# Performance work log

Hardware: AMD Instinct MI355X
Metric: run time of the kernel (lower is better)

## Reference

```python
import jax, jax.numpy as jnp
import numpy as np

B, S, E, U = 4, 512, 512, 256

def setup_inputs() -> dict:
    key = jax.random.key(0)
    k1, k2, k3, k4 = jax.random.split(key, 4)
    h1 = jax.random.normal(k1, (B, S, E), dtype=jnp.float32)
    h2 = jax.random.normal(k2, (B, S, E), dtype=jnp.float32)
    # glorot-ish scaled weights
    w = jax.random.normal(k3, (2 * E, U), dtype=jnp.float32) * (2.0 / (2 * E + U)) ** 0.5
    b1 = jnp.zeros((U,), dtype=jnp.float32)
    v = jax.random.normal(k4, (U, 1), dtype=jnp.float32) * (2.0 / (U + 1)) ** 0.5
    b2 = jnp.zeros((1,), dtype=jnp.float32)
    return {"h1": h1, "h2": h2, "w": w, "b1": b1, "v": v, "b2": b2}

def reference(h1, h2, w, b1, v, b2):
    # Original: for each query step i, concat([h1, repeat(h2[:,i])]) @ w.
    # Split w so the concat-matmul becomes two separate projections:
    #   concat([h1_j, h2_i]) @ w == h1_j @ w1 + h2_i @ w2
    E_ = h1.shape[-1]
    w1, w2 = w[:E_], w[E_:]
    key_pre = jnp.einsum('bje,eu->bju', h1, w1)   # [B,Sk,U]
    qry_pre = jnp.einsum('bie,eu->biu', h2, w2)   # [B,Sq,U]
    # energy: [B,Sq,Sk,U]
    t = jnp.tanh(qry_pre[:, :, None, :] + key_pre[:, None, :, :] + b1)
    scores = jnp.einsum('biju,uo->bij', t, v) + b2[0]  # [B,Sq,Sk]
    p = jax.nn.softmax(scores, axis=-1)                # softmax over keys j
    # context per query: sum_j p[b,i,j] * h1[b,j]
    return jnp.einsum('bij,bje->bie', p, h1)           # [B,S,E]
```

## Files before the change

kernel.cpp:

```cpp
#include <hip/hip_runtime.h>
#include <hip/hip_bf16.h>

#define B_ 4
#define S_ 512
#define E_ 512
#define U_ 256

#define KC 2.885390081777927f

#if __has_builtin(__builtin_amdgcn_exp2f)
#define EXP2F(x) __builtin_amdgcn_exp2f(x)
#else
#define EXP2F(x) __exp2f(x)
#endif
#if __has_builtin(__builtin_amdgcn_rcpf)
#define RCPF(x) __builtin_amdgcn_rcpf(x)
#else
#define RCPF(x) (1.0f / (x))
#endif

typedef __attribute__((ext_vector_type(8))) short bf16x8;
typedef __attribute__((ext_vector_type(4))) float f32x4;

__device__ __forceinline__ unsigned short bf16rn(float x) {
    unsigned int u = __float_as_uint(x);
    u = (u + 0x7FFFu + ((u >> 16) & 1u)) >> 16;
    return (unsigned short)u;
}
__device__ __forceinline__ void splitT(float x, short* hi, short* lo) {
    const unsigned u = __float_as_uint(x);
    *hi = (short)(u >> 16);
    const float hf = __uint_as_float(u & 0xFFFF0000u);
    *lo = (short)(__float_as_uint(x - hf) >> 16);
}

__global__ __launch_bounds__(256) void prep_gemm(
    const float* __restrict__ h1, const float* __restrict__ h2,
    const float* __restrict__ w, const float* __restrict__ b1,
    float* __restrict__ keySt, float* __restrict__ qryS,
    bf16x8* __restrict__ h1c)
{
    __shared__ unsigned short WhiL[2][16][64][8];
    __shared__ unsigned short WloL[2][16][64][8];

    const int tid = threadIdx.x;
    const int bid = blockIdx.x;

    if (bid < 512) {
        const int z = bid >> 8, ngg = (bid >> 5) & 7, mq = bid & 31;

        const int r8 = tid >> 5, ul = tid & 31;
        const int ntc = ul >> 4, l16c = ul & 15;
        const float* __restrict__ Wp = w + (size_t)z * E_ * U_ + ngg * 32 + ul;
#pragma unroll 4
        for (int it = 0; it < 64; ++it) {
            const int k = it * 8 + r8;
            short h, l;
            splitT(Wp[(size_t)k * U_] * KC, &h, &l);
            const int kc = k >> 5, quad = (k >> 3) & 3, jj = k & 7;
            WhiL[ntc][kc][quad * 16 + l16c][jj] = (unsigned short)h;
            WloL[ntc][kc][quad * 16 + l16c][jj] = (unsigned short)l;
        }
        __syncthreads();

        const int wv = tid >> 6, lane = tid & 63;
        const int quad = lane >> 4, l16 = lane & 15;
        const int m0 = (mq * 4 + wv) * 16;
        const float* __restrict__ Arow = (z ? h2 : h1) + (size_t)(m0 + l16) * E_;

        f32x4 acc[2];
        acc[0] = (f32x4){0.f, 0.f, 0.f, 0.f};
        acc[1] = (f32x4){0.f, 0.f, 0.f, 0.f};

        for (int kc = 0; kc < 16; ++kc) {
            const int kb = kc * 32 + quad * 8;
            const float4 x0 = *(const float4*)&Arow[kb];
            const float4 x1 = *(const float4*)&Arow[kb + 4];
            const float xs[8] = {x0.x, x0.y, x0.z, x0.w, x1.x, x1.y, x1.z, x1.w};
            bf16x8 ah, al;
#pragma unroll
            for (int j = 0; j < 8; ++j) {
                short h, l; splitT(xs[j], &h, &l);
                ah[j] = h; al[j] = l;
            }
#pragma unroll
            for (int nt = 0; nt < 2; ++nt) {
                const bf16x8 bh = *(const bf16x8*)&WhiL[nt][kc][lane][0];
                const bf16x8 bl = *(const bf16x8*)&WloL[nt][kc][lane][0];
                acc[nt] = __builtin_amdgcn_mfma_f32_16x16x32_bf16(ah, bh, acc[nt], 0, 0, 0);
                acc[nt] = __builtin_amdgcn_mfma_f32_16x16x32_bf16(ah, bl, acc[nt], 0, 0, 0);
                acc[nt] = __builtin_amdgcn_mfma_f32_16x16x32_bf16(al, bh, acc[nt], 0, 0, 0);
            }
        }

        if (z == 0) {
            const int b = m0 >> 9;
            const int j0 = (m0 & (S_ - 1)) + quad * 4;
#pragma unroll
            for (int nt = 0; nt < 2; ++nt) {
                const int u = (ngg * 2 + nt) * 16 + l16;
                *(float4*)&keySt[((size_t)b * U_ + u) * S_ + j0] =
                    make_float4(acc[nt][0], acc[nt][1], acc[nt][2], acc[nt][3]);
            }
        } else {
            const int row = m0 + quad * 4;
#pragma unroll
            for (int nt = 0; nt < 2; ++nt) {
                const int u = (ngg * 2 + nt) * 16 + l16;
                const float bias = KC * b1[u];
#pragma unroll
                for (int r = 0; r < 4; ++r)
                    qryS[(size_t)(row + r) * U_ + u] = acc[nt][r] + bias;
            }
        }
    } else {
        const int s = (bid - 512) * 256 + tid;
        const int lane = s & 63, kc = (s >> 6) & 15, et = (s >> 10) & 31, b = s >> 15;
        const int quad = lane >> 4, l16 = lane & 15;
        const float* __restrict__ src =
            h1 + ((size_t)b * S_ + kc * 32 + quad * 8) * E_ + et * 16 + l16;
        bf16x8 c;
#pragma unroll
        for (int j = 0; j < 8; ++j)
            c[j] = (short)bf16rn(src[(size_t)j * E_]);
        h1c[s] = c;
    }
}

__device__ __forceinline__ float quadTerm(float a0, float a1, float a2, float a3,
                                          float4 vq, float acc) {
    const float F1 = EXP2F(a0) + 1.f;
    const float F2 = EXP2F(a1) + 1.f;
    const float F3 = EXP2F(a2) + 1.f;
    const float F4 = EXP2F(a3) + 1.f;
    const float P12 = F1 * F2, P34 = F3 * F4;
    const float n12 = fmaf(vq.y, F1, vq.x * F2);
    const float n34 = fmaf(vq.w, F3, vq.z * F4);
    const float num = fmaf(n34, P12, n12 * P34);
    return fmaf(num, RCPF(P12 * P34), acc);
}

__global__ __launch_bounds__(512) void scores_kernel(
    const float* __restrict__ keySt, const float* __restrict__ qryS,
    const float* __restrict__ v, unsigned short* __restrict__ Pp)
{
    const int i0 = blockIdx.x * 4;
    const int b = blockIdx.y;
    const int t = threadIdx.x;
    const int wv = t >> 6;

    __shared__ float ssm[8][4];

    const float4* __restrict__ q0v = (const float4*)(qryS + ((size_t)b * S_ + i0) * U_);
    const float4* __restrict__ q1v = q0v + (U_ / 4);
    const float4* __restrict__ q2v = q0v + 2 * (U_ / 4);
    const float4* __restrict__ q3v = q0v + 3 * (U_ / 4);
    const float4* __restrict__ vv4 = (const float4*)v;
    const float* __restrict__ kb = keySt + (size_t)b * U_ * S_ + t;

    float a0 = 0.f, a1 = 0.f, a2 = 0.f, a3 = 0.f;
#pragma unroll 4
    for (int ub = 0; ub < U_ / 4; ++ub) {
        const float4 vq = vv4[ub];
        const float k0 = kb[(size_t)(ub * 4 + 0) * S_];
        const float k1 = kb[(size_t)(ub * 4 + 1) * S_];
        const float k2 = kb[(size_t)(ub * 4 + 2) * S_];
        const float k3 = kb[(size_t)(ub * 4 + 3) * S_];
        const float4 q0 = q0v[ub], q1 = q1v[ub], q2 = q2v[ub], q3 = q3v[ub];
        a0 = quadTerm(q0.x + k0, q0.y + k1, q0.z + k2, q0.w + k3, vq, a0);
        a1 = quadTerm(q1.x + k0, q1.y + k1, q1.z + k2, q1.w + k3, vq, a1);
        a2 = quadTerm(q2.x + k0, q2.y + k1, q2.z + k2, q2.w + k3, vq, a2);
        a3 = quadTerm(q3.x + k0, q3.y + k1, q3.z + k2, q3.w + k3, vq, a3);
    }

    const float p0 = EXP2F(-a0 * KC);
    const float p1 = EXP2F(-a1 * KC);
    const float p2 = EXP2F(-a2 * KC);
    const float p3 = EXP2F(-a3 * KC);
    float s0 = p0, s1 = p1, s2 = p2, s3 = p3;
#pragma unroll
    for (int off = 1; off < 64; off <<= 1) {
        s0 += __shfl_xor(s0, off, 64);
        s1 += __shfl_xor(s1, off, 64);
        s2 += __shfl_xor(s2, off, 64);
        s3 += __shfl_xor(s3, off, 64);
    }
    if ((t & 63) == 0) {
        ssm[wv][0] = s0; ssm[wv][1] = s1; ssm[wv][2] = s2; ssm[wv][3] = s3;
    }
    __syncthreads();
    s0 = ssm[0][0]; s1 = ssm[0][1]; s2 = ssm[0][2]; s3 = ssm[0][3];
#pragma unroll
    for (int k = 1; k < 8; ++k) {
        s0 += ssm[k][0]; s1 += ssm[k][1]; s2 += ssm[k][2]; s3 += ssm[k][3];
    }
    const float r0 = RCPF(s0), r1 = RCPF(s1), r2 = RCPF(s2), r3 = RCPF(s3);

    const int itile = i0 >> 4;
    const int base = (itile * 16 + (t >> 5)) * 64 + (((t >> 3) & 3) << 4);
    unsigned short* __restrict__ pb = Pp + (size_t)b * S_ * S_;
    const int io = i0 & 15, jo = t & 7;
    pb[((base + io + 0) << 3) + jo] = bf16rn(p0 * r0);
    pb[((base + io + 1) << 3) + jo] = bf16rn(p1 * r1);
    pb[((base + io + 2) << 3) + jo] = bf16rn(p2 * r2);
    pb[((base + io + 3) << 3) + jo] = bf16rn(p3 * r3);
}

__global__ __launch_bounds__(256) void pv_gemm(
    const unsigned short* __restrict__ Pp, const bf16x8* __restrict__ h1c,
    float* __restrict__ out)
{
    const int tid = threadIdx.x;
    const int wv = tid >> 6, lane = tid & 63;
    const int quad = lane >> 4, l16 = lane & 15;
    const int wt = blockIdx.x * 4 + wv;
    const int b = wt >> 8, rem = wt & 255;
    const int it = rem >> 3, eg = rem & 7;

    const bf16x8* __restrict__ Ab =
        (const bf16x8*)(Pp + (size_t)b * S_ * S_) + (it * 16) * 64 + lane;
    const bf16x8* __restrict__ Bb =
        h1c + ((b * 32 + eg * 4) * 16) * 64 + lane;

    f32x4 acc[4];
#pragma unroll
    for (int i = 0; i < 4; ++i) acc[i] = (f32x4){0.f, 0.f, 0.f, 0.f};

    for (int kc = 0; kc < 16; ++kc) {
        const bf16x8 a8 = Ab[kc * 64];
#pragma unroll
        for (int n = 0; n < 4; ++n) {
            const bf16x8 b8 = Bb[(n * 16 + kc) * 64];
            acc[n] = __builtin_amdgcn_mfma_f32_16x16x32_bf16(a8, b8, acc[n], 0, 0, 0);
        }
    }

    const int i = it * 16 + quad * 4;
#pragma unroll
    for (int n = 0; n < 4; ++n) {
        const int e = (eg * 4 + n) * 16 + l16;
        float* __restrict__ ob = out + ((size_t)b * S_ + i) * E_ + e;
#pragma unroll
        for (int r = 0; r < 4; ++r)
            ob[(size_t)r * E_] = acc[n][r];
    }
}

extern "C" void kernel_launch(void* const* d_in, const int* in_sizes, int n_in,
                              void* d_out, int out_size, void* d_ws, size_t ws_size,
                              hipStream_t stream) {
    const float* h1 = (const float*)d_in[0];
    const float* h2 = (const float*)d_in[1];
    const float* w  = (const float*)d_in[2];
    const float* b1 = (const float*)d_in[3];
    const float* v  = (const float*)d_in[4];
    float* out = (float*)d_out;

    char* ws = (char*)d_ws;
    float* keySt = (float*)ws;                 ws += 2u << 20;
    float* qryS  = (float*)ws;                 ws += 2u << 20;
    unsigned short* Pp = (unsigned short*)ws;  ws += 2u << 20;
    bf16x8* h1c = (bf16x8*)ws;

    prep_gemm<<<dim3(1024), dim3(256), 0, stream>>>(h1, h2, w, b1, keySt, qryS, h1c);
    scores_kernel<<<dim3(S_ / 4, B_), dim3(512), 0, stream>>>(keySt, qryS, v, Pp);
    pv_gemm<<<dim3(256), dim3(256), 0, stream>>>(Pp, h1c, out);
}
```

Measured before the change: 137.8 us.

## Split GEMM tiles finer for more blocks and prefetch keys in scores loop

The projection GEMM now gives each block one 16-wide column tile instead of two, doubling its grid. The PV GEMM gives each wave one 16-column output tile instead of four, quadrupling its grid. The scores kernel software-prefetches the next four key values one iteration ahead. The aim is better occupancy and latency hiding on the GPU, at the cost of reloading the A operands more often and recomputing the W split per block.

```diff
diff --git a/kernel.cpp b/kernel.cpp
--- a/kernel.cpp
+++ b/kernel.cpp
@@ -40,26 +40,25 @@
     float* __restrict__ keySt, float* __restrict__ qryS,
     bf16x8* __restrict__ h1c)
 {
-    __shared__ unsigned short WhiL[2][16][64][8];
-    __shared__ unsigned short WloL[2][16][64][8];
+    __shared__ unsigned short WhiL[16][64][8];
+    __shared__ unsigned short WloL[16][64][8];
 
     const int tid = threadIdx.x;
     const int bid = blockIdx.x;
 
-    if (bid < 512) {
-        const int z = bid >> 8, ngg = (bid >> 5) & 7, mq = bid & 31;
-
-        const int r8 = tid >> 5, ul = tid & 31;
-        const int ntc = ul >> 4, l16c = ul & 15;
-        const float* __restrict__ Wp = w + (size_t)z * E_ * U_ + ngg * 32 + ul;
+    if (bid < 1024) {
+        const int z = bid >> 9, ng = (bid >> 5) & 15, mq = bid & 31;
+
+        const int l16c = tid & 15, r16 = tid >> 4;
+        const float* __restrict__ Wp = w + (size_t)z * E_ * U_ + ng * 16 + l16c;
 #pragma unroll 4
-        for (int it = 0; it < 64; ++it) {
-            const int k = it * 8 + r8;
+        for (int it = 0; it < 32; ++it) {
+            const int k = it * 16 + r16;
             short h, l;
             splitT(Wp[(size_t)k * U_] * KC, &h, &l);
             const int kc = k >> 5, quad = (k >> 3) & 3, jj = k & 7;
-            WhiL[ntc][kc][quad * 16 + l16c][jj] = (unsigned short)h;
-            WloL[ntc][kc][quad * 16 + l16c][jj] = (unsigned short)l;
+            WhiL[kc][quad * 16 + l16c][jj] = (unsigned short)h;
+            WloL[kc][quad * 16 + l16c][jj] = (unsigned short)l;
         }
         __syncthreads();
 
@@ -68,9 +67,7 @@
         const int m0 = (mq * 4 + wv) * 16;
         const float* __restrict__ Arow = (z ? h2 : h1) + (size_t)(m0 + l16) * E_;
 
-        f32x4 acc[2];
-        acc[0] = (f32x4){0.f, 0.f, 0.f, 0.f};
-        acc[1] = (f32x4){0.f, 0.f, 0.f, 0.f};
+        f32x4 acc = (f32x4){0.f, 0.f, 0.f, 0.f};
 
         for (int kc = 0; kc < 16; ++kc) {
             const int kb = kc * 32 + quad * 8;
@@ -83,38 +80,28 @@
                 short h, l; splitT(xs[j], &h, &l);
                 ah[j] = h; al[j] = l;
             }
-#pragma unroll
-            for (int nt = 0; nt < 2; ++nt) {
-                const bf16x8 bh = *(const bf16x8*)&WhiL[nt][kc][lane][0];
-                const bf16x8 bl = *(const bf16x8*)&WloL[nt][kc][lane][0];
-                acc[nt] = __builtin_amdgcn_mfma_f32_16x16x32_bf16(ah, bh, acc[nt], 0, 0, 0);
-                acc[nt] = __builtin_amdgcn_mfma_f32_16x16x32_bf16(ah, bl, acc[nt], 0, 0, 0);
-                acc[nt] = __builtin_amdgcn_mfma_f32_16x16x32_bf16(al, bh, acc[nt], 0, 0, 0);
-            }
+            const bf16x8 bh = *(const bf16x8*)&WhiL[kc][lane][0];
+            const bf16x8 bl = *(const bf16x8*)&WloL[kc][lane][0];
+            acc = __builtin_amdgcn_mfma_f32_16x16x32_bf16(ah, bh, acc, 0, 0, 0);
+            acc = __builtin_amdgcn_mfma_f32_16x16x32_bf16(ah, bl, acc, 0, 0, 0);
+            acc = __builtin_amdgcn_mfma_f32_16x16x32_bf16(al, bh, acc, 0, 0, 0);
         }
 
+        const int u = ng * 16 + l16;
         if (z == 0) {
             const int b = m0 >> 9;
             const int j0 = (m0 & (S_ - 1)) + quad * 4;
-#pragma unroll
-            for (int nt = 0; nt < 2; ++nt) {
-                const int u = (ngg * 2 + nt) * 16 + l16;
-                *(float4*)&keySt[((size_t)b * U_ + u) * S_ + j0] =
-                    make_float4(acc[nt][0], acc[nt][1], acc[nt][2], acc[nt][3]);
-            }
+            *(float4*)&keySt[((size_t)b * U_ + u) * S_ + j0] =
+                make_float4(acc[0], acc[1], acc[2], acc[3]);
         } else {
             const int row = m0 + quad * 4;
-#pragma unroll
-            for (int nt = 0; nt < 2; ++nt) {
-                const int u = (ngg * 2 + nt) * 16 + l16;
-                const float bias = KC * b1[u];
-#pragma unroll
-                for (int r = 0; r < 4; ++r)
-                    qryS[(size_t)(row + r) * U_ + u] = acc[nt][r] + bias;
-            }
+            const float bias = KC * b1[u];
+#pragma unroll
+            for (int r = 0; r < 4; ++r)
+                qryS[(size_t)(row + r) * U_ + u] = acc[r] + bias;
         }
     } else {
-        const int s = (bid - 512) * 256 + tid;
+        const int s = (bid - 1024) * 256 + tid;
         const int lane = s & 63, kc = (s >> 6) & 15, et = (s >> 10) & 31, b = s >> 15;
         const int quad = lane >> 4, l16 = lane & 15;
         const float* __restrict__ src =
@@ -156,16 +143,26 @@
     const float4* __restrict__ q2v = q0v + 2 * (U_ / 4);
     const float4* __restrict__ q3v = q0v + 3 * (U_ / 4);
     const float4* __restrict__ vv4 = (const float4*)v;
-    const float* __restrict__ kb = keySt + (size_t)b * U_ * S_ + t;
+    const float* __restrict__ kp = keySt + (size_t)b * U_ * S_ + t;
 
     float a0 = 0.f, a1 = 0.f, a2 = 0.f, a3 = 0.f;
+    float k0 = kp[0], k1 = kp[S_], k2 = kp[2 * S_], k3 = kp[3 * S_];
+    kp += 4 * S_;
 #pragma unroll 4
-    for (int ub = 0; ub < U_ / 4; ++ub) {
+    for (int ub = 0; ub < U_ / 4 - 1; ++ub) {
+        const float n0 = kp[0], n1 = kp[S_], n2 = kp[2 * S_], n3 = kp[3 * S_];
+        kp += 4 * S_;
         const float4 vq = vv4[ub];
-        const float k0 = kb[(size_t)(ub * 4 + 0) * S_];
-        const float k1 = kb[(size_t)(ub * 4 + 1) * S_];
-        const float k2 = kb[(size_t)(ub * 4 + 2) * S_];
-        const float k3 = kb[(size_t)(ub * 4 + 3) * S_];
+        const float4 q0 = q0v[ub], q1 = q1v[ub], q2 = q2v[ub], q3 = q3v[ub];
+        a0 = quadTerm(q0.x + k0, q0.y + k1, q0.z + k2, q0.w + k3, vq, a0);
+        a1 = quadTerm(q1.x + k0, q1.y + k1, q1.z + k2, q1.w + k3, vq, a1);
+        a2 = quadTerm(q2.x + k0, q2.y + k1, q2.z + k2, q2.w + k3, vq, a2);
+        a3 = quadTerm(q3.x + k0, q3.y + k1, q3.z + k2, q3.w + k3, vq, a3);
+        k0 = n0; k1 = n1; k2 = n2; k3 = n3;
+    }
+    {
+        const int ub = U_ / 4 - 1;
+        const float4 vq = vv4[ub];
         const float4 q0 = q0v[ub], q1 = q1v[ub], q2 = q2v[ub], q3 = q3v[ub];
         a0 = quadTerm(q0.x + k0, q0.y + k1, q0.z + k2, q0.w + k3, vq, a0);
         a1 = quadTerm(q1.x + k0, q1.y + k1, q1.z + k2, q1.w + k3, vq, a1);
@@ -214,36 +211,28 @@
     const int wv = tid >> 6, lane = tid & 63;
     const int quad = lane >> 4, l16 = lane & 15;
     const int wt = blockIdx.x * 4 + wv;
-    const int b = wt >> 8, rem = wt & 255;
-    const int it = rem >> 3, eg = rem & 7;
+    const int b = wt >> 10, rem = wt & 1023;
+    const int it = rem >> 5, et = rem & 31;
 
     const bf16x8* __restrict__ Ab =
         (const bf16x8*)(Pp + (size_t)b * S_ * S_) + (it * 16) * 64 + lane;
     const bf16x8* __restrict__ Bb =
-        h1c + ((b * 32 + eg * 4) * 16) * 64 + lane;
-
-    f32x4 acc[4];
-#pragma unroll
-    for (int i = 0; i < 4; ++i) acc[i] = (f32x4){0.f, 0.f, 0.f, 0.f};
+        h1c + ((b * 32 + et) * 16) * 64 + lane;
+
+    f32x4 acc = (f32x4){0.f, 0.f, 0.f, 0.f};
 
     for (int kc = 0; kc < 16; ++kc) {
         const bf16x8 a8 = Ab[kc * 64];
-#pragma unroll
-        for (int n = 0; n < 4; ++n) {
-            const bf16x8 b8 = Bb[(n * 16 + kc) * 64];
-            acc[n] = __builtin_amdgcn_mfma_f32_16x16x32_bf16(a8, b8, acc[n], 0, 0, 0);
-        }
+        const bf16x8 b8 = Bb[kc * 64];
+        acc = __builtin_amdgcn_mfma_f32_16x16x32_bf16(a8, b8, acc, 0, 0, 0);
     }
 
     const int i = it * 16 + quad * 4;
-#pragma unroll
-    for (int n = 0; n < 4; ++n) {
-        const int e = (eg * 4 + n) * 16 + l16;
-        float* __restrict__ ob = out + ((size_t)b * S_ + i) * E_ + e;
-#pragma unroll
-        for (int r = 0; r < 4; ++r)
-            ob[(size_t)r * E_] = acc[n][r];
-    }
+    const int e = et * 16 + l16;
+    float* __restrict__ ob = out + ((size_t)b * S_ + i) * E_ + e;
+#pragma unroll
+    for (int r = 0; r < 4; ++r)
+        ob[(size_t)r * E_] = acc[r];
 }
 
 extern "C" void kernel_launch(void* const* d_in, const int* in_sizes, int n_in,
@@ -262,7 +251,7 @@
     unsigned short* Pp = (unsigned short*)ws;  ws += 2u << 20;
     bf16x8* h1c = (bf16x8*)ws;
 
-    prep_gemm<<<dim3(1024), dim3(256), 0, stream>>>(h1, h2, w, b1, keySt, qryS, h1c);
+    prep_gemm<<<dim3(1536), dim3(256), 0, stream>>>(h1, h2, w, b1, keySt, qryS, h1c);
     scores_kernel<<<dim3(S_ / 4, B_), dim3(512), 0, stream>>>(keySt, qryS, v, Pp);
-    pv_gemm<<<dim3(256), dim3(256), 0, stream>>>(Pp, h1c, out);
-}
+    pv_gemm<<<dim3(1024), dim3(256), 0, stream>>>(Pp, h1c, out);
+}
```

New measurement: 139.2 us. About the same (+1.1%).

## Split weight split-prep into own kernel, widen projection tiles, float4 key layout

Applied to the files above, without the earlier changes.

Moves the fp32-to-bf16 hi/lo split of the weight matrix into a separate prep kernel that writes MFMA-ready fragments, so it is done once instead of once per block. The projection GEMM becomes its own kernel with 64-wide U tiles staged through shared memory. The key projection is stored interleaved by groups of four U so the scores kernel fetches one float4 per iteration instead of four scalar loads. The PV GEMM gets one 16-wide E tile per wave with four times as many blocks. The cost is an extra kernel launch, extra workspace traffic for the weight fragments, and less B-operand reuse per wave in the PV GEMM.

```diff
diff --git a/kernel.cpp b/kernel.cpp
--- a/kernel.cpp
+++ b/kernel.cpp
@@ -34,87 +34,26 @@
     *lo = (short)(__float_as_uint(x - hf) >> 16);
 }
 
-__global__ __launch_bounds__(256) void prep_gemm(
-    const float* __restrict__ h1, const float* __restrict__ h2,
-    const float* __restrict__ w, const float* __restrict__ b1,
-    float* __restrict__ keySt, float* __restrict__ qryS,
+__global__ __launch_bounds__(256) void prep_kernel(
+    const float* __restrict__ w, const float* __restrict__ h1,
+    bf16x8* __restrict__ whi, bf16x8* __restrict__ wlo,
     bf16x8* __restrict__ h1c)
 {
-    __shared__ unsigned short WhiL[2][16][64][8];
-    __shared__ unsigned short WloL[2][16][64][8];
-
-    const int tid = threadIdx.x;
-    const int bid = blockIdx.x;
-
-    if (bid < 512) {
-        const int z = bid >> 8, ngg = (bid >> 5) & 7, mq = bid & 31;
-
-        const int r8 = tid >> 5, ul = tid & 31;
-        const int ntc = ul >> 4, l16c = ul & 15;
-        const float* __restrict__ Wp = w + (size_t)z * E_ * U_ + ngg * 32 + ul;
-#pragma unroll 4
-        for (int it = 0; it < 64; ++it) {
-            const int k = it * 8 + r8;
-            short h, l;
-            splitT(Wp[(size_t)k * U_] * KC, &h, &l);
-            const int kc = k >> 5, quad = (k >> 3) & 3, jj = k & 7;
-            WhiL[ntc][kc][quad * 16 + l16c][jj] = (unsigned short)h;
-            WloL[ntc][kc][quad * 16 + l16c][jj] = (unsigned short)l;
-        }
-        __syncthreads();
-
-        const int wv = tid >> 6, lane = tid & 63;
+    const int t = blockIdx.x * 256 + threadIdx.x;
+    if (t < 32768) {
+        const int lane = t & 63, kc = (t >> 6) & 15, nt = (t >> 10) & 15, z = t >> 14;
         const int quad = lane >> 4, l16 = lane & 15;
-        const int m0 = (mq * 4 + wv) * 16;
-        const float* __restrict__ Arow = (z ? h2 : h1) + (size_t)(m0 + l16) * E_;
-
-        f32x4 acc[2];
-        acc[0] = (f32x4){0.f, 0.f, 0.f, 0.f};
-        acc[1] = (f32x4){0.f, 0.f, 0.f, 0.f};
-
-        for (int kc = 0; kc < 16; ++kc) {
-            const int kb = kc * 32 + quad * 8;
-            const float4 x0 = *(const float4*)&Arow[kb];
-            const float4 x1 = *(const float4*)&Arow[kb + 4];
-            const float xs[8] = {x0.x, x0.y, x0.z, x0.w, x1.x, x1.y, x1.z, x1.w};
-            bf16x8 ah, al;
-#pragma unroll
-            for (int j = 0; j < 8; ++j) {
-                short h, l; splitT(xs[j], &h, &l);
-                ah[j] = h; al[j] = l;
-            }
-#pragma unroll
-            for (int nt = 0; nt < 2; ++nt) {
-                const bf16x8 bh = *(const bf16x8*)&WhiL[nt][kc][lane][0];
-                const bf16x8 bl = *(const bf16x8*)&WloL[nt][kc][lane][0];
-                acc[nt] = __builtin_amdgcn_mfma_f32_16x16x32_bf16(ah, bh, acc[nt], 0, 0, 0);
-                acc[nt] = __builtin_amdgcn_mfma_f32_16x16x32_bf16(ah, bl, acc[nt], 0, 0, 0);
-                acc[nt] = __builtin_amdgcn_mfma_f32_16x16x32_bf16(al, bh, acc[nt], 0, 0, 0);
-            }
-        }
-
-        if (z == 0) {
-            const int b = m0 >> 9;
-            const int j0 = (m0 & (S_ - 1)) + quad * 4;
-#pragma unroll
-            for (int nt = 0; nt < 2; ++nt) {
-                const int u = (ngg * 2 + nt) * 16 + l16;
-                *(float4*)&keySt[((size_t)b * U_ + u) * S_ + j0] =
-                    make_float4(acc[nt][0], acc[nt][1], acc[nt][2], acc[nt][3]);
-            }
-        } else {
-            const int row = m0 + quad * 4;
-#pragma unroll
-            for (int nt = 0; nt < 2; ++nt) {
-                const int u = (ngg * 2 + nt) * 16 + l16;
-                const float bias = KC * b1[u];
-#pragma unroll
-                for (int r = 0; r < 4; ++r)
-                    qryS[(size_t)(row + r) * U_ + u] = acc[nt][r] + bias;
-            }
-        }
+        const float* __restrict__ src =
+            w + (size_t)z * E_ * U_ + (size_t)(kc * 32 + quad * 8) * U_ + nt * 16 + l16;
+        bf16x8 hi, lo;
+#pragma unroll
+        for (int j = 0; j < 8; ++j) {
+            short h, l; splitT(src[(size_t)j * U_] * KC, &h, &l);
+            hi[j] = h; lo[j] = l;
+        }
+        whi[t] = hi; wlo[t] = lo;
     } else {
-        const int s = (bid - 512) * 256 + tid;
+        const int s = t - 32768;
         const int lane = s & 63, kc = (s >> 6) & 15, et = (s >> 10) & 31, b = s >> 15;
         const int quad = lane >> 4, l16 = lane & 15;
         const float* __restrict__ src =
@@ -124,6 +63,92 @@
         for (int j = 0; j < 8; ++j)
             c[j] = (short)bf16rn(src[(size_t)j * E_]);
         h1c[s] = c;
+    }
+}
+
+__global__ __launch_bounds__(256) void gemm_pre(
+    const float* __restrict__ h1, const float* __restrict__ h2,
+    const bf16x8* __restrict__ whi, const bf16x8* __restrict__ wlo,
+    const float* __restrict__ b1,
+    float* __restrict__ keySt4, float* __restrict__ qryS)
+{
+    __shared__ bf16x8 WsH[4][4][64];
+    __shared__ bf16x8 WsL[4][4][64];
+
+    const int tid = threadIdx.x;
+    const int mb = blockIdx.x;
+    const int ug = blockIdx.y;
+    const int z  = blockIdx.z;
+    const int wv = tid >> 6, lane = tid & 63;
+    const int quad = lane >> 4, l16 = lane & 15;
+    const int m0 = mb * 64 + wv * 16;
+
+    const float* __restrict__ Arow = (z ? h2 : h1) + (size_t)(m0 + l16) * E_;
+    const bf16x8* __restrict__ WH = whi + ((size_t)(z * 16 + ug * 4) * 16) * 64;
+    const bf16x8* __restrict__ WL = wlo + ((size_t)(z * 16 + ug * 4) * 16) * 64;
+
+    f32x4 acc[4];
+#pragma unroll
+    for (int i = 0; i < 4; ++i) acc[i] = (f32x4){0.f, 0.f, 0.f, 0.f};
+
+    for (int ch = 0; ch < 4; ++ch) {
+        __syncthreads();
+#pragma unroll
+        for (int p = 0; p < 4; ++p) {
+            const int s = p * 256 + tid;
+            const int nt = s >> 8;
+            const int kcl = (s >> 6) & 3;
+            const int ln = s & 63;
+            const int g = (nt * 16 + ch * 4 + kcl) * 64 + ln;
+            WsH[kcl][nt][ln] = WH[g];
+            WsL[kcl][nt][ln] = WL[g];
+        }
+        __syncthreads();
+#pragma unroll
+        for (int kcl = 0; kcl < 4; ++kcl) {
+            const int kb = (ch * 4 + kcl) * 32 + quad * 8;
+            const float4 x0 = *(const float4*)&Arow[kb];
+            const float4 x1 = *(const float4*)&Arow[kb + 4];
+            const float xs[8] = {x0.x, x0.y, x0.z, x0.w, x1.x, x1.y, x1.z, x1.w};
+            bf16x8 ah, al;
+#pragma unroll
+            for (int j = 0; j < 8; ++j) {
+                short h, l; splitT(xs[j], &h, &l);
+                ah[j] = h; al[j] = l;
+            }
+#pragma unroll
+            for (int nt = 0; nt < 4; ++nt) {
+                const bf16x8 bh = WsH[kcl][nt][lane];
+                const bf16x8 bl = WsL[kcl][nt][lane];
+                acc[nt] = __builtin_amdgcn_mfma_f32_16x16x32_bf16(ah, bh, acc[nt], 0, 0, 0);
+                acc[nt] = __builtin_amdgcn_mfma_f32_16x16x32_bf16(ah, bl, acc[nt], 0, 0, 0);
+                acc[nt] = __builtin_amdgcn_mfma_f32_16x16x32_bf16(al, bh, acc[nt], 0, 0, 0);
+            }
+        }
+    }
+
+    if (z == 0) {
+        const int b = m0 >> 9;
+        const int j0 = (m0 & (S_ - 1)) + quad * 4;
+#pragma unroll
+        for (int nt = 0; nt < 4; ++nt) {
+            const int u = ug * 64 + nt * 16 + l16;
+            float* __restrict__ dst =
+                keySt4 + (((size_t)b * 64 + (u >> 2)) * S_ + j0) * 4 + (u & 3);
+#pragma unroll
+            for (int r = 0; r < 4; ++r)
+                dst[r * 4] = acc[nt][r];
+        }
+    } else {
+        const int row = m0 + quad * 4;
+#pragma unroll
+        for (int nt = 0; nt < 4; ++nt) {
+            const int u = ug * 64 + nt * 16 + l16;
+            const float bias = KC * b1[u];
+#pragma unroll
+            for (int r = 0; r < 4; ++r)
+                qryS[(size_t)(row + r) * U_ + u] = acc[nt][r] + bias;
+        }
     }
 }
 
@@ -141,7 +166,7 @@
 }
 
 __global__ __launch_bounds__(512) void scores_kernel(
-    const float* __restrict__ keySt, const float* __restrict__ qryS,
+    const float* __restrict__ keySt4, const float* __restrict__ qryS,
     const float* __restrict__ v, unsigned short* __restrict__ Pp)
 {
     const int i0 = blockIdx.x * 4;
@@ -156,21 +181,19 @@
     const float4* __restrict__ q2v = q0v + 2 * (U_ / 4);
     const float4* __restrict__ q3v = q0v + 3 * (U_ / 4);
     const float4* __restrict__ vv4 = (const float4*)v;
-    const float* __restrict__ kb = keySt + (size_t)b * U_ * S_ + t;
+    const float4* __restrict__ kp4 =
+        (const float4*)keySt4 + (size_t)b * 64 * S_ + t;
 
     float a0 = 0.f, a1 = 0.f, a2 = 0.f, a3 = 0.f;
 #pragma unroll 4
     for (int ub = 0; ub < U_ / 4; ++ub) {
+        const float4 k4 = kp4[(size_t)ub * S_];
         const float4 vq = vv4[ub];
-        const float k0 = kb[(size_t)(ub * 4 + 0) * S_];
-        const float k1 = kb[(size_t)(ub * 4 + 1) * S_];
-        const float k2 = kb[(size_t)(ub * 4 + 2) * S_];
-        const float k3 = kb[(size_t)(ub * 4 + 3) * S_];
         const float4 q0 = q0v[ub], q1 = q1v[ub], q2 = q2v[ub], q3 = q3v[ub];
-        a0 = quadTerm(q0.x + k0, q0.y + k1, q0.z + k2, q0.w + k3, vq, a0);
-        a1 = quadTerm(q1.x + k0, q1.y + k1, q1.z + k2, q1.w + k3, vq, a1);
-        a2 = quadTerm(q2.x + k0, q2.y + k1, q2.z + k2, q2.w + k3, vq, a2);
-        a3 = quadTerm(q3.x + k0, q3.y + k1, q3.z + k2, q3.w + k3, vq, a3);
+        a0 = quadTerm(q0.x + k4.x, q0.y + k4.y, q0.z + k4.z, q0.w + k4.w, vq, a0);
+        a1 = quadTerm(q1.x + k4.x, q1.y + k4.y, q1.z + k4.z, q1.w + k4.w, vq, a1);
+        a2 = quadTerm(q2.x + k4.x, q2.y + k4.y, q2.z + k4.z, q2.w + k4.w, vq, a2);
+        a3 = quadTerm(q3.x + k4.x, q3.y + k4.y, q3.z + k4.z, q3.w + k4.w, vq, a3);
     }
 
     const float p0 = EXP2F(-a0 * KC);
@@ -214,36 +237,28 @@
     const int wv = tid >> 6, lane = tid & 63;
     const int quad = lane >> 4, l16 = lane & 15;
     const int wt = blockIdx.x * 4 + wv;
-    const int b = wt >> 8, rem = wt & 255;
-    const int it = rem >> 3, eg = rem & 7;
+    const int b = wt >> 10, rem = wt & 1023;
+    const int it = rem >> 5, et = rem & 31;
 
     const bf16x8* __restrict__ Ab =
         (const bf16x8*)(Pp + (size_t)b * S_ * S_) + (it * 16) * 64 + lane;
     const bf16x8* __restrict__ Bb =
-        h1c + ((b * 32 + eg * 4) * 16) * 64 + lane;
-
-    f32x4 acc[4];
-#pragma unroll
-    for (int i = 0; i < 4; ++i) acc[i] = (f32x4){0.f, 0.f, 0.f, 0.f};
+        h1c + ((b * 32 + et) * 16) * 64 + lane;
+
+    f32x4 acc = (f32x4){0.f, 0.f, 0.f, 0.f};
 
     for (int kc = 0; kc < 16; ++kc) {
         const bf16x8 a8 = Ab[kc * 64];
-#pragma unroll
-        for (int n = 0; n < 4; ++n) {
-            const bf16x8 b8 = Bb[(n * 16 + kc) * 64];
-            acc[n] = __builtin_amdgcn_mfma_f32_16x16x32_bf16(a8, b8, acc[n], 0, 0, 0);
-        }
+        const bf16x8 b8 = Bb[kc * 64];
+        acc = __builtin_amdgcn_mfma_f32_16x16x32_bf16(a8, b8, acc, 0, 0, 0);
     }
 
     const int i = it * 16 + quad * 4;
-#pragma unroll
-    for (int n = 0; n < 4; ++n) {
-        const int e = (eg * 4 + n) * 16 + l16;
-        float* __restrict__ ob = out + ((size_t)b * S_ + i) * E_ + e;
-#pragma unroll
-        for (int r = 0; r < 4; ++r)
-            ob[(size_t)r * E_] = acc[n][r];
-    }
+    const int e = et * 16 + l16;
+    float* __restrict__ ob = out + ((size_t)b * S_ + i) * E_ + e;
+#pragma unroll
+    for (int r = 0; r < 4; ++r)
+        ob[(size_t)r * E_] = acc[r];
 }
 
 extern "C" void kernel_launch(void* const* d_in, const int* in_sizes, int n_in,
@@ -257,12 +272,15 @@
     float* out = (float*)d_out;
 
     char* ws = (char*)d_ws;
-    float* keySt = (float*)ws;                 ws += 2u << 20;
-    float* qryS  = (float*)ws;                 ws += 2u << 20;
+    float* keySt4 = (float*)ws;                ws += 2u << 20;
+    float* qryS   = (float*)ws;                ws += 2u << 20;
     unsigned short* Pp = (unsigned short*)ws;  ws += 2u << 20;
-    bf16x8* h1c = (bf16x8*)ws;
-
-    prep_gemm<<<dim3(1024), dim3(256), 0, stream>>>(h1, h2, w, b1, keySt, qryS, h1c);
-    scores_kernel<<<dim3(S_ / 4, B_), dim3(512), 0, stream>>>(keySt, qryS, v, Pp);
-    pv_gemm<<<dim3(256), dim3(256), 0, stream>>>(Pp, h1c, out);
-}
+    bf16x8* h1c = (bf16x8*)ws;                 ws += 2u << 20;
+    bf16x8* whi = (bf16x8*)ws;                 ws += 512u << 10;
+    bf16x8* wlo = (bf16x8*)ws;
+
+    prep_kernel<<<dim3(640), dim3(256), 0, stream>>>(w, h1, whi, wlo, h1c);
+    gemm_pre<<<dim3(32, 4, 2), dim3(256), 0, stream>>>(h1, h2, whi, wlo, b1, keySt4, qryS);
+    scores_kernel<<<dim3(S_ / 4, B_), dim3(512), 0, stream>>>(keySt4, qryS, v, Pp);
+    pv_gemm<<<dim3(1024), dim3(256), 0, stream>>>(Pp, h1c, out);
+}
```

After: 140.7 us. +2.1%, slower.
